# Kernel tuning notes

Measured on AMD Instinct MI355X. Metric: run time of the kernel, lower is better.

## Reference

```python
import jax, jax.numpy as jnp
import numpy as np

B, NT, NC, NN = 2, 64, 1024, 1024
C, H = 1024, 16
HD = C // H
N = NT + NC + NN
EPS = 1e-5
NEG = -1e30


def _ln(t, w, b):
    # LayerNorm over last dim (head_dim), torch eps=1e-5
    mu = jnp.mean(t, axis=-1, keepdims=True)
    var = jnp.mean(jnp.square(t - mu), axis=-1, keepdims=True)
    return (t - mu) * jax.lax.rsqrt(var + EPS) * w + b


def _rope(q, k, pos):
    # q,k: [B,H,S,HD]; pos: [B,S]; rotate-half RoPE, base 10000
    hd = q.shape[-1]
    half = hd // 2
    inv_freq = 1.0 / (10000.0 ** (jnp.arange(half, dtype=jnp.float32) / half))
    ang = pos.astype(jnp.float32)[:, None, :, None] * inv_freq  # [B,1,S,half]
    cos, sin = jnp.cos(ang), jnp.sin(ang)
    def rot(t):
        t1, t2 = t[..., :half], t[..., half:]
        return jnp.concatenate([t1 * cos - t2 * sin, t2 * cos + t1 * sin], axis=-1)
    return rot(q), rot(k)


def setup_inputs() -> dict:
    key = jax.random.key(0)
    ks = jax.random.split(key, 4)
    s = 0.02
    return {
        "x": jax.random.normal(ks[0], (B, N, C), jnp.float32),
        "position_ids": jnp.broadcast_to(jnp.arange(NC + NN, dtype=jnp.int32), (B, NC + NN)),
        "text_position_ids": jnp.broadcast_to(jnp.arange(NT, dtype=jnp.int32), (B, NT)),
        "attention_mask": jnp.tril(jnp.ones((N, N), dtype=bool)),
        "n_text": NT, "n_clean": NC, "n_noised": NN,
        "qkv_w": jax.random.normal(ks[1], (3, 3 * C, C), jnp.float32) * s,
        "qkv_b": jnp.zeros((3, 3 * C), jnp.float32),
        "qn_w": jnp.ones((3, HD), jnp.float32),
        "qn_b": jnp.zeros((3, HD), jnp.float32),
        "kn_w": jnp.ones((3, HD), jnp.float32),
        "kn_b": jnp.zeros((3, HD), jnp.float32),
        "proj_w": jax.random.normal(ks[2], (3, C, C), jnp.float32) * s,
        "proj_b": jnp.zeros((3, C), jnp.float32),
    }


def reference(x, position_ids, text_position_ids, attention_mask, n_text, n_clean, n_noised,
              qkv_w, qkv_b, qn_w, qn_b, kn_w, kn_b, proj_w, proj_b):
    Bx, Nx, Cx = x.shape
    hd = qn_w.shape[-1]
    nh = Cx // hd
    b0, b1 = n_text, n_text + n_clean
    segs = (x[:, :b0], x[:, b0:b1], x[:, b1:])  # text / clean / noised

    qs, kks, vvs = [], [], []
    for i, xs in enumerate(segs):
        S = xs.shape[1]
        qkv = jnp.einsum('bsc,oc->bso', xs, qkv_w[i]) + qkv_b[i]
        qkv = qkv.reshape(Bx, S, 3, nh, hd).transpose(2, 0, 3, 1, 4)  # [3,B,H,S,hd]
        q = _ln(qkv[0], qn_w[i], qn_b[i])
        k = _ln(qkv[1], kn_w[i], kn_b[i])
        qs.append(q); kks.append(k); vvs.append(qkv[2])

    img_q = jnp.concatenate([qs[1], qs[2]], axis=2)
    img_k = jnp.concatenate([kks[1], kks[2]], axis=2)
    img_q, img_k = _rope(img_q, img_k, position_ids)
    txt_q, txt_k = _rope(qs[0], kks[0], text_position_ids)

    q = jnp.concatenate([txt_q, img_q], axis=2)
    k = jnp.concatenate([txt_k, img_k], axis=2)
    v = jnp.concatenate(vvs, axis=2)

    scale = 1.0 / np.sqrt(hd).astype(np.float32)
    scores = jnp.einsum('bhqd,bhkd->bhqk', q, k) * scale
    scores = jnp.where(attention_mask, scores, NEG)
    attn = jax.nn.softmax(scores, axis=-1)
    out = jnp.einsum('bhqk,bhkd->bhqd', attn, v)
    out = out.transpose(0, 2, 1, 3).reshape(Bx, Nx, Cx)

    o_segs = (out[:, :b0], out[:, b0:b1], out[:, b1:])
    outs = [jnp.einsum('bsc,oc->bso', o_segs[i], proj_w[i]) + proj_b[i] for i in range(3)]
    return jnp.concatenate(outs, axis=1)
```

## Files before the change

### kernel.cpp

```cpp
#include <hip/hip_runtime.h>
#include <hip/hip_bf16.h>

#define BB   2
#define NT   64
#define NC   1024
#define NN   1024
#define NTOK (NT + NC + NN)
#define CC   1024
#define HH   16
#define HD   64
#define K3   (3 * CC)
#define EPSV 1e-5f

typedef __attribute__((ext_vector_type(8))) short short8;
typedef __attribute__((ext_vector_type(4))) float f32x4;
typedef __attribute__((ext_vector_type(4))) float float4v;

__device__ __forceinline__ short bf16raw(float x) {
    __hip_bfloat16 h = __float2bfloat16(x);
    return *(short*)&h;
}

#define GL_LDS(gptr, lptr) \
    __builtin_amdgcn_global_load_lds( \
        (const __attribute__((address_space(1))) void*)(gptr), \
        (__attribute__((address_space(3))) void*)(lptr), 16, 0, 0)

__constant__ signed char QB_tab[33] =
    {16,16,16,15,15,15,14,14,14,13,13,13,12,12,12,11,11,10,10,9,9,8,8,7,7,6,6,5,4,3,2,1,0};
__constant__ signed char CH_tab[33] =
    { 0, 1, 2, 0, 1, 2, 0, 1, 2, 0, 1, 2, 0, 1, 2, 0, 1, 0, 1,0,1,0,1,0,1,0,1,0,0,0,0,0,0};

__global__ __launch_bounds__(256) void cast_all(
    const float* __restrict__ s0, const float* __restrict__ s1, const float* __restrict__ s2,
    __hip_bfloat16* __restrict__ d0, __hip_bfloat16* __restrict__ d1, __hip_bfloat16* __restrict__ d2,
    int n0, int n1, int n2)
{
    int i = blockIdx.x * 256 + threadIdx.x;
    int stride = gridDim.x * 256;
    int ntot = n0 + n1 + n2;
    for (; i < ntot; i += stride) {
        const float* sp; short* dp; int j;
        if (i < n0)            { sp = s0; dp = (short*)d0; j = i; }
        else if (i < n0 + n1)  { sp = s1; dp = (short*)d1; j = i - n0; }
        else                   { sp = s2; dp = (short*)d2; j = i - n0 - n1; }
        float4v v = *(const float4v*)(sp + (size_t)j * 4);
        short4 o;
        o.x = bf16raw(v.x); o.y = bf16raw(v.y); o.z = bf16raw(v.z); o.w = bf16raw(v.w);
        *(short4*)(dp + (size_t)j * 4) = o;
    }
}

__global__ __launch_bounds__(256) void gemm_qkv(
    const __hip_bfloat16* __restrict__ A,
    const __hip_bfloat16* __restrict__ Wb,
    const float* __restrict__ biasb,
    const float* __restrict__ qn_w, const float* __restrict__ qn_b,
    const float* __restrict__ kn_w, const float* __restrict__ kn_b,
    __hip_bfloat16* __restrict__ Q,
    __hip_bfloat16* __restrict__ Kg,
    __hip_bfloat16* __restrict__ Vt)
{
    __shared__ short buf[128 * 134];
    short* As = buf;
    short* Bs = buf + 8192;

    int tid = threadIdx.x;
    int lane = tid & 63, w = tid >> 6;
    int l15 = lane & 15, quad = lane >> 4;
    int wm = w >> 1, wn = w & 1;
    int r7 = l15 & 7;

    int y = blockIdx.y;
    int seg, tm;
    if (y < 16)      { seg = 1; tm = y * 128; }
    else if (y < 32) { seg = 2; tm = (y - 16) * 128; }
    else             { seg = 0; tm = 0; }
    int S = (seg == 0) ? 64 : 1024;
    int seg_start = (seg == 0) ? 0 : (seg == 1 ? NT : NT + NC);
    const short* W = (const short*)Wb + (size_t)seg * K3 * CC;
    const float* bias = biasb + (size_t)seg * K3;
    int tileN = blockIdx.x * 128;

    const short* aptr[4];
    const short* bptr[4];
#pragma unroll
    for (int j = 0; j < 4; ++j) {
        int c = j * 256 + tid;
        int row = c >> 3, u = (c & 7) ^ (row & 7);
        int ar = tm + row;
        int arow = (ar / S) * NTOK + seg_start + (ar % S);
        aptr[j] = (const short*)A + (size_t)arow * CC + u * 8;
        bptr[j] = W + (size_t)(tileN + row) * CC + u * 8;
    }

    f32x4 zero = {0.f, 0.f, 0.f, 0.f};
    f32x4 acc[4][4];
#pragma unroll
    for (int mb = 0; mb < 4; ++mb)
#pragma unroll
        for (int nb = 0; nb < 4; ++nb) acc[mb][nb] = zero;

    for (int k0 = 0; k0 < CC; k0 += 64) {
        __syncthreads();
#pragma unroll
        for (int j = 0; j < 4; ++j) {
            int c8 = (j * 256 + tid) * 8;
            GL_LDS(aptr[j] + k0, As + c8);
            GL_LDS(bptr[j] + k0, Bs + c8);
        }
        __syncthreads();

#pragma unroll
        for (int s = 0; s < 2; ++s) {
            int sx = ((s * 4 + quad) ^ r7) * 8;
            short8 af[4], bf[4];
#pragma unroll
            for (int mb = 0; mb < 4; ++mb)
                af[mb] = *(const short8*)&As[(wm * 64 + mb * 16 + l15) * 64 + sx];
#pragma unroll
            for (int nb = 0; nb < 4; ++nb)
                bf[nb] = *(const short8*)&Bs[(wn * 64 + nb * 16 + l15) * 64 + sx];
#pragma unroll
            for (int mb = 0; mb < 4; ++mb)
#pragma unroll
                for (int nb = 0; nb < 4; ++nb)
                    acc[mb][nb] = __builtin_amdgcn_mfma_f32_16x16x32_bf16(af[mb], bf[nb], acc[mb][nb], 0, 0, 0);
        }
    }

    int sect = tileN >> 10;
    __syncthreads();

    if (sect < 2) {
        const float* nw = (sect == 0 ? qn_w : kn_w) + seg * HD;
        const float* nbv = (sect == 0 ? qn_b : kn_b) + seg * HD;
        float lw[4], lb[4], bcol[4];
#pragma unroll
        for (int nb = 0; nb < 4; ++nb) {
            lw[nb] = nw[nb * 16 + l15];
            lb[nb] = nbv[nb * 16 + l15];
            bcol[nb] = bias[tileN + wn * 64 + nb * 16 + l15];
        }
        float qscale = (sect == 0) ? 0.125f : 1.0f;

        float invf0 = expf(-9.210340371976184f * (float)l15 * (1.0f / 32.0f));
        float invf1 = expf(-9.210340371976184f * (float)(16 + l15) * (1.0f / 32.0f));
        float cd0, sd0, cd1, sd1;
        sincosf(invf0, &sd0, &cd0);
        sincosf(invf1, &sd1, &cd1);

#pragma unroll
        for (int mb = 0; mb < 4; ++mb) {
            int tok0 = wm * 64 + mb * 16 + quad * 4;
            int ar0 = tm + tok0;
            int nloc0 = ar0 % S;
            int pos0 = (seg == 0) ? nloc0 : (seg_start + nloc0 - NT);
            float c0, s0, c1, s1v;
            sincosf((float)pos0 * invf0, &s0, &c0);
            sincosf((float)pos0 * invf1, &s1v, &c1);

#pragma unroll
            for (int r = 0; r < 4; ++r) {
                int tok = tok0 + r;
                float v[4];
#pragma unroll
                for (int nb = 0; nb < 4; ++nb) v[nb] = acc[mb][nb][r] + bcol[nb];

                float t1 = v[0] + v[1] + v[2] + v[3];
                float t2 = v[0] * v[0] + v[1] * v[1] + v[2] * v[2] + v[3] * v[3];
#pragma unroll
                for (int off = 8; off >= 1; off >>= 1) {
                    t1 += __shfl_xor(t1, off);
                    t2 += __shfl_xor(t2, off);
                }
                float mu = t1 * (1.0f / 64.0f);
                float var = t2 * (1.0f / 64.0f) - mu * mu;
                float rstd = rsqrtf(var + EPSV);
#pragma unroll
                for (int nb = 0; nb < 4; ++nb) v[nb] = (v[nb] - mu) * rstd * lw[nb] + lb[nb];

                short* bp = &buf[tok * 134 + wn * 64];
                bp[0 * 16 + l15] = bf16raw((v[0] * c0 - v[2] * s0) * qscale);
                bp[1 * 16 + l15] = bf16raw((v[1] * c1 - v[3] * s1v) * qscale);
                bp[2 * 16 + l15] = bf16raw((v[2] * c0 + v[0] * s0) * qscale);
                bp[3 * 16 + l15] = bf16raw((v[3] * c1 + v[1] * s1v) * qscale);

                float nc0 = c0 * cd0 - s0 * sd0, ns0 = s0 * cd0 + c0 * sd0;
                float nc1 = c1 * cd1 - s1v * sd1, ns1 = s1v * cd1 + c1 * sd1;
                c0 = nc0; s0 = ns0; c1 = nc1; s1v = ns1;
            }
        }
        __syncthreads();
        __hip_bfloat16* dst = (sect == 0) ? Q : Kg;
        int head_base = (tileN & 1023) >> 6;
#pragma unroll
        for (int it = 0; it < 8; ++it) {
            int idx = it * 256 + tid;
            int tok = idx >> 4, cc = (idx & 15) * 8;
            int ar = tm + tok;
            int bb = ar / S;
            int nloc = seg_start + (ar % S);
            int hh2 = head_base + (cc >> 6), d = cc & 63;
            *(short8*)((short*)dst + ((size_t)(bb * HH + hh2) * NTOK + nloc) * HD + d) =
                *(const short8*)&buf[tok * 134 + cc];
        }
    } else {
        float bcol[4];
#pragma unroll
        for (int nb = 0; nb < 4; ++nb) bcol[nb] = bias[tileN + wn * 64 + nb * 16 + l15];
#pragma unroll
        for (int mb = 0; mb < 4; ++mb) {
#pragma unroll
            for (int r = 0; r < 4; ++r) {
                int tok = wm * 64 + mb * 16 + quad * 4 + r;
#pragma unroll
                for (int nb = 0; nb < 4; ++nb) {
                    int col = wn * 64 + nb * 16 + l15;
                    buf[col * 134 + tok] = bf16raw(acc[mb][nb][r] + bcol[nb]);
                }
            }
        }
        __syncthreads();
#pragma unroll
        for (int it = 0; it < 8; ++it) {
            int idx = it * 256 + tid;
            int row = idx >> 4;
            int tc = (idx & 15) * 8;
            int vcol = (tileN - 2048) + row;
            int h = vcol >> 6, d = vcol & 63;
            int ar = tm + tc;
            int bb = ar / S;
            int nloc = seg_start + (ar % S);
            short8 val = *(const short8*)&buf[row * 134 + tc];
            *(short8*)((short*)Vt + ((size_t)(bb * HH + h) * HD + d) * NTOK + nloc) = val;
        }
    }
}

__global__ __launch_bounds__(256) void gemm_proj(
    const __hip_bfloat16* __restrict__ A,
    const __hip_bfloat16* __restrict__ Wb,
    const float* __restrict__ biasb,
    float* __restrict__ Cout)
{
    __shared__ short As[64 * 64];
    __shared__ short Bs[128 * 64];

    int tid = threadIdx.x;
    int lane = tid & 63, w = tid >> 6;
    int l15 = lane & 15, quad = lane >> 4;
    int wm = w >> 1, wn = w & 1;
    int r7 = l15 & 7;

    int y = blockIdx.y;
    int seg, tm;
    if (y < 32)      { seg = 1; tm = y * 64; }
    else if (y < 64) { seg = 2; tm = (y - 32) * 64; }
    else             { seg = 0; tm = (y - 64) * 64; }
    int S = (seg == 0) ? 64 : 1024;
    int seg_start = (seg == 0) ? 0 : (seg == 1 ? NT : NT + NC);
    const short* W = (const short*)Wb + (size_t)seg * CC * CC;
    const float* bias = biasb + (size_t)seg * CC;
    int tileN = blockIdx.x * 128;

    const short* aptr[2];
    const short* bptr[4];
#pragma unroll
    for (int j = 0; j < 2; ++j) {
        int c = j * 256 + tid;
        int row = c >> 3, u = (c & 7) ^ (row & 7);
        int ar = tm + row;
        int arow = (ar / S) * NTOK + seg_start + (ar % S);
        aptr[j] = (const short*)A + (size_t)arow * CC + u * 8;
    }
#pragma unroll
    for (int j = 0; j < 4; ++j) {
        int c = j * 256 + tid;
        int row = c >> 3, u = (c & 7) ^ (row & 7);
        bptr[j] = W + (size_t)(tileN + row) * CC + u * 8;
    }

    f32x4 zero = {0.f, 0.f, 0.f, 0.f};
    f32x4 acc[2][4];
#pragma unroll
    for (int mb = 0; mb < 2; ++mb)
#pragma unroll
        for (int nb = 0; nb < 4; ++nb) acc[mb][nb] = zero;

    for (int k0 = 0; k0 < CC; k0 += 64) {
        __syncthreads();
#pragma unroll
        for (int j = 0; j < 2; ++j)
            GL_LDS(aptr[j] + k0, As + (j * 256 + tid) * 8);
#pragma unroll
        for (int j = 0; j < 4; ++j)
            GL_LDS(bptr[j] + k0, Bs + (j * 256 + tid) * 8);
        __syncthreads();

#pragma unroll
        for (int s = 0; s < 2; ++s) {
            int sx = ((s * 4 + quad) ^ r7) * 8;
            short8 af[2], bf[4];
#pragma unroll
            for (int mb = 0; mb < 2; ++mb)
                af[mb] = *(const short8*)&As[(wm * 32 + mb * 16 + l15) * 64 + sx];
#pragma unroll
            for (int nb = 0; nb < 4; ++nb)
                bf[nb] = *(const short8*)&Bs[(wn * 64 + nb * 16 + l15) * 64 + sx];
#pragma unroll
            for (int mb = 0; mb < 2; ++mb)
#pragma unroll
                for (int nb = 0; nb < 4; ++nb)
                    acc[mb][nb] = __builtin_amdgcn_mfma_f32_16x16x32_bf16(af[mb], bf[nb], acc[mb][nb], 0, 0, 0);
        }
    }

#pragma unroll
    for (int mb = 0; mb < 2; ++mb) {
#pragma unroll
        for (int r = 0; r < 4; ++r) {
            int ar = tm + wm * 32 + mb * 16 + quad * 4 + r;
            int crow = (ar / S) * NTOK + seg_start + (ar % S);
            float* cp = Cout + (size_t)crow * CC + tileN;
#pragma unroll
            for (int nb = 0; nb < 4; ++nb) {
                int col = wn * 64 + nb * 16 + l15;
                cp[col] = acc[mb][nb][r] + bias[tileN + col];
            }
        }
    }
}

__global__ __launch_bounds__(512) void attn_part(
    const __hip_bfloat16* __restrict__ Q,
    const __hip_bfloat16* __restrict__ Kg,
    const __hip_bfloat16* __restrict__ Vt,
    __hip_bfloat16* __restrict__ O,
    float* __restrict__ Opart,
    float* __restrict__ lpart)
{
    __shared__ short Ks[64 * 64];
    __shared__ short Vs[64 * 64];
    __shared__ short Ps[8][16 * 72];

    int tid = threadIdx.x;
    int lane = tid & 63, w = tid >> 6;
    int quad = lane >> 4, l15 = lane & 15;
    int r7 = l15 & 7;
    int bh = blockIdx.y, b = bh >> 4, h = bh & 15;

    int e = blockIdx.x;
    int qb = QB_tab[e], c = CH_tab[e];
    int q0 = qb * 128;
    int nt = 2 * qb + 2; if (nt > 33) nt = 33;
    int t0 = c * 12, t1 = t0 + 12; if (t1 > nt) t1 = nt;
    bool direct = (nt <= 12);

    size_t base = (size_t)bh * NTOK * HD;

    int qrow = q0 + w * 16 + l15;
    int qr_c = qrow < NTOK ? qrow : NTOK - 1;
    short8 qf0 = *(const short8*)((const short*)Q + base + (size_t)qr_c * HD + quad * 8);
    short8 qf1 = *(const short8*)((const short*)Q + base + (size_t)qr_c * HD + 32 + quad * 8);

    int srow = tid >> 3;
    int su = (tid & 7) ^ (srow & 7);
    const short* kptr = (const short*)Kg + base + (size_t)srow * HD + su * 8;
    const short* vptr = (const short*)Vt + base + (size_t)srow * NTOK + su * 8;
    int c8 = tid * 8;

    f32x4 zero = {0.f, 0.f, 0.f, 0.f};
    f32x4 oacc[4] = {zero, zero, zero, zero};
    float l[4] = {0.f, 0.f, 0.f, 0.f};

    int qmax_w = q0 + w * 16 + 15;
    int sx0 = (quad ^ r7) * 8;
    int sx1 = ((4 + quad) ^ r7) * 8;

    for (int t = t0; t < t1; ++t) {
        __syncthreads();
        GL_LDS(kptr + (size_t)(t * 64) * HD, Ks + c8);
        GL_LDS(vptr + t * 64, Vs + c8);
        __syncthreads();
        if (t * 64 > qmax_w) continue;

        f32x4 s[4];
#pragma unroll
        for (int kb = 0; kb < 4; ++kb) {
            int krow = (kb * 16 + l15) * 64;
            short8 kf0 = *(const short8*)&Ks[krow + sx0];
            short8 kf1 = *(const short8*)&Ks[krow + sx1];
            f32x4 z = zero;
            z = __builtin_amdgcn_mfma_f32_16x16x32_bf16(qf0, kf0, z, 0, 0, 0);
            z = __builtin_amdgcn_mfma_f32_16x16x32_bf16(qf1, kf1, z, 0, 0, 0);
            s[kb] = z;
        }

#pragma unroll
        for (int r = 0; r < 4; ++r) {
            int qg = q0 + w * 16 + quad * 4 + r;
#pragma unroll
            for (int kb = 0; kb < 4; ++kb) {
                int kgk = t * 64 + kb * 16 + l15;
                float p = (kgk <= qg) ? __expf(s[kb][r]) : 0.f;
                Ps[w][(quad * 4 + r) * 72 + kb * 16 + l15] = bf16raw(p);
                l[r] += p;
            }
        }

        __builtin_amdgcn_wave_barrier();

#pragma unroll
        for (int sl = 0; sl < 2; ++sl) {
            short8 pf = *(const short8*)&Ps[w][l15 * 72 + sl * 32 + quad * 8];
            int vsx = ((sl * 4 + quad) ^ r7) * 8;
#pragma unroll
            for (int db = 0; db < 4; ++db) {
                short8 vf = *(const short8*)&Vs[(db * 16 + l15) * 64 + vsx];
                oacc[db] = __builtin_amdgcn_mfma_f32_16x16x32_bf16(pf, vf, oacc[db], 0, 0, 0);
            }
        }
    }

#pragma unroll
    for (int r = 0; r < 4; ++r) {
#pragma unroll
        for (int off = 8; off >= 1; off >>= 1) l[r] += __shfl_xor(l[r], off);
    }

    if (direct) {
#pragma unroll
        for (int r = 0; r < 4; ++r) {
            int qg = q0 + w * 16 + quad * 4 + r;
            float inv_l = 1.0f / l[r];
#pragma unroll
            for (int db = 0; db < 4; ++db) {
                O[(size_t)(b * NTOK + qg) * CC + h * HD + db * 16 + l15] =
                    __float2bfloat16(oacc[db][r] * inv_l);
            }
        }
    } else {
        int pidx = (bh * 17 + qb) * 3 + c;
        float* op = Opart + (size_t)pidx * (128 * 64);
#pragma unroll
        for (int r = 0; r < 4; ++r) {
            int q = w * 16 + quad * 4 + r;
#pragma unroll
            for (int db = 0; db < 4; ++db)
                op[q * 64 + db * 16 + l15] = oacc[db][r];
            if (l15 == 0) lpart[pidx * 128 + q] = l[r];
        }
    }
}

__global__ __launch_bounds__(512) void attn_comb(
    const float* __restrict__ Opart, const float* __restrict__ lpart,
    __hip_bfloat16* __restrict__ O)
{
    __shared__ float ls[128];
    int tid = threadIdx.x;
    int qb = 6 + blockIdx.x;
    int bh = blockIdx.y, b = bh >> 4, h = bh & 15;
    int nt = 2 * qb + 2; if (nt > 33) nt = 33;
    int nch = (nt + 11) / 12;
    int q0 = qb * 128;
    int pbase = (bh * 17 + qb) * 3;

    if (tid < 128) {
        float s = 0.f;
        for (int cc = 0; cc < nch; ++cc) s += lpart[(pbase + cc) * 128 + tid];
        ls[tid] = 1.0f / s;
    }
    __syncthreads();

#pragma unroll
    for (int k = 0; k < 16; ++k) {
        int elem = k * 512 + tid;
        int q = elem >> 6, d = elem & 63;
        int qg = q0 + q;
        if (qg >= NTOK) continue;
        float s = 0.f;
        for (int cc = 0; cc < nch; ++cc)
            s += Opart[(size_t)(pbase + cc) * (128 * 64) + elem];
        O[(size_t)(b * NTOK + qg) * CC + h * HD + d] = __float2bfloat16(s * ls[q]);
    }
}

extern "C" void kernel_launch(void* const* d_in, const int* in_sizes, int n_in,
                              void* d_out, int out_size, void* d_ws, size_t ws_size,
                              hipStream_t stream) {
    const float* x      = (const float*)d_in[0];
    const float* qkv_w  = (const float*)d_in[7];
    const float* qkv_b  = (const float*)d_in[8];
    const float* qn_w   = (const float*)d_in[9];
    const float* qn_b   = (const float*)d_in[10];
    const float* kn_w   = (const float*)d_in[11];
    const float* kn_b   = (const float*)d_in[12];
    const float* proj_w = (const float*)d_in[13];
    const float* proj_b = (const float*)d_in[14];
    float* out = (float*)d_out;

    const size_t n_x    = (size_t)BB * NTOK * CC;
    const size_t n_qkvw = (size_t)3 * K3 * CC;
    const size_t n_prjw = (size_t)3 * CC * CC;
    const size_t n_part = (size_t)32 * 17 * 3;

    __hip_bfloat16* x_bf    = (__hip_bfloat16*)d_ws;
    __hip_bfloat16* qkvw_bf = x_bf + n_x;
    __hip_bfloat16* prjw_bf = qkvw_bf + n_qkvw;
    __hip_bfloat16* Qbf  = prjw_bf + n_prjw;
    __hip_bfloat16* Kbf  = Qbf + n_x;
    __hip_bfloat16* Vtbf = Kbf + n_x;
    float* Opart = (float*)(Vtbf + n_x);
    float* lpart = Opart + n_part * (128 * 64);
    __hip_bfloat16* attn_bf = x_bf;

    cast_all<<<1024, 256, 0, stream>>>(x, qkv_w, proj_w, x_bf, qkvw_bf, prjw_bf,
                                       (int)(n_x / 4), (int)(n_qkvw / 4), (int)(n_prjw / 4));

    gemm_qkv<<<dim3(K3 / 128, 33), 256, 0, stream>>>(
        x_bf, qkvw_bf, qkv_b,
        qn_w, qn_b, kn_w, kn_b, Qbf, Kbf, Vtbf);

    attn_part<<<dim3(33, BB * HH), 512, 0, stream>>>(Qbf, Kbf, Vtbf, attn_bf, Opart, lpart);

    attn_comb<<<dim3(11, BB * HH), 512, 0, stream>>>(Opart, lpart, attn_bf);

    gemm_proj<<<dim3(CC / 128, 66), 256, 0, stream>>>(attn_bf, prjw_bf, proj_b, out);
}
```

Baseline: 270.6 us.

## Double-buffer LDS tiles in QKV, projection and attention kernels

Adds ping-pong LDS buffers to the QKV GEMM, projection GEMM and attention loop. The next K-tile (or K/V block) is issued with global_load_lds before computing on the current one, and the two barriers per iteration become one. This is meant to hide global-load latency behind MFMA work. LDS use doubles per block, which may lower occupancy, most notably in the QKV GEMM at 64KB.

```diff
diff --git a/kernel.cpp b/kernel.cpp
--- a/kernel.cpp
+++ b/kernel.cpp
@@ -61,9 +61,8 @@
     __hip_bfloat16* __restrict__ Kg,
     __hip_bfloat16* __restrict__ Vt)
 {
-    __shared__ short buf[128 * 134];
-    short* As = buf;
-    short* Bs = buf + 8192;
+    __shared__ short lds[32768];
+    short* buf = lds;
 
     int tid = threadIdx.x;
     int lane = tid & 63, w = tid >> 6;
@@ -101,15 +100,27 @@
 #pragma unroll
         for (int nb = 0; nb < 4; ++nb) acc[mb][nb] = zero;
 
-    for (int k0 = 0; k0 < CC; k0 += 64) {
-        __syncthreads();
-#pragma unroll
-        for (int j = 0; j < 4; ++j) {
-            int c8 = (j * 256 + tid) * 8;
-            GL_LDS(aptr[j] + k0, As + c8);
-            GL_LDS(bptr[j] + k0, Bs + c8);
-        }
-        __syncthreads();
+#pragma unroll
+    for (int j = 0; j < 4; ++j) {
+        int c8 = (j * 256 + tid) * 8;
+        GL_LDS(aptr[j], lds + c8);
+        GL_LDS(bptr[j], lds + 8192 + c8);
+    }
+    __syncthreads();
+
+    int cur = 0;
+    for (int k0 = 64; k0 <= CC; k0 += 64) {
+        short* As = lds + cur * 16384;
+        short* Bs = As + 8192;
+        if (k0 < CC) {
+            short* An = lds + (cur ^ 1) * 16384;
+#pragma unroll
+            for (int j = 0; j < 4; ++j) {
+                int c8 = (j * 256 + tid) * 8;
+                GL_LDS(aptr[j] + k0, An + c8);
+                GL_LDS(bptr[j] + k0, An + 8192 + c8);
+            }
+        }
 
 #pragma unroll
         for (int s = 0; s < 2; ++s) {
@@ -127,10 +138,11 @@
                 for (int nb = 0; nb < 4; ++nb)
                     acc[mb][nb] = __builtin_amdgcn_mfma_f32_16x16x32_bf16(af[mb], bf[nb], acc[mb][nb], 0, 0, 0);
         }
+        __syncthreads();
+        cur ^= 1;
     }
 
     int sect = tileN >> 10;
-    __syncthreads();
 
     if (sect < 2) {
         const float* nw = (sect == 0 ? qn_w : kn_w) + seg * HD;
@@ -244,8 +256,7 @@
     const float* __restrict__ biasb,
     float* __restrict__ Cout)
 {
-    __shared__ short As[64 * 64];
-    __shared__ short Bs[128 * 64];
+    __shared__ short lds[24576];
 
     int tid = threadIdx.x;
     int lane = tid & 63, w = tid >> 6;
@@ -288,15 +299,27 @@
 #pragma unroll
         for (int nb = 0; nb < 4; ++nb) acc[mb][nb] = zero;
 
-    for (int k0 = 0; k0 < CC; k0 += 64) {
-        __syncthreads();
-#pragma unroll
-        for (int j = 0; j < 2; ++j)
-            GL_LDS(aptr[j] + k0, As + (j * 256 + tid) * 8);
-#pragma unroll
-        for (int j = 0; j < 4; ++j)
-            GL_LDS(bptr[j] + k0, Bs + (j * 256 + tid) * 8);
-        __syncthreads();
+#pragma unroll
+    for (int j = 0; j < 2; ++j)
+        GL_LDS(aptr[j], lds + (j * 256 + tid) * 8);
+#pragma unroll
+    for (int j = 0; j < 4; ++j)
+        GL_LDS(bptr[j], lds + 4096 + (j * 256 + tid) * 8);
+    __syncthreads();
+
+    int cur = 0;
+    for (int k0 = 64; k0 <= CC; k0 += 64) {
+        short* As = lds + cur * 12288;
+        short* Bs = As + 4096;
+        if (k0 < CC) {
+            short* An = lds + (cur ^ 1) * 12288;
+#pragma unroll
+            for (int j = 0; j < 2; ++j)
+                GL_LDS(aptr[j] + k0, An + (j * 256 + tid) * 8);
+#pragma unroll
+            for (int j = 0; j < 4; ++j)
+                GL_LDS(bptr[j] + k0, An + 4096 + (j * 256 + tid) * 8);
+        }
 
 #pragma unroll
         for (int s = 0; s < 2; ++s) {
@@ -314,6 +337,8 @@
                 for (int nb = 0; nb < 4; ++nb)
                     acc[mb][nb] = __builtin_amdgcn_mfma_f32_16x16x32_bf16(af[mb], bf[nb], acc[mb][nb], 0, 0, 0);
         }
+        __syncthreads();
+        cur ^= 1;
     }
 
 #pragma unroll
@@ -340,8 +365,8 @@
     float* __restrict__ Opart,
     float* __restrict__ lpart)
 {
-    __shared__ short Ks[64 * 64];
-    __shared__ short Vs[64 * 64];
+    __shared__ short Ks[2][4096];
+    __shared__ short Vs[2][4096];
     __shared__ short Ps[8][16 * 72];
 
     int tid = threadIdx.x;
@@ -378,49 +403,58 @@
     int sx0 = (quad ^ r7) * 8;
     int sx1 = ((4 + quad) ^ r7) * 8;
 
+    GL_LDS(kptr + (size_t)(t0 * 64) * HD, Ks[0] + c8);
+    GL_LDS(vptr + t0 * 64, Vs[0] + c8);
+    __syncthreads();
+
+    int cur = 0;
     for (int t = t0; t < t1; ++t) {
+        if (t + 1 < t1) {
+            GL_LDS(kptr + (size_t)((t + 1) * 64) * HD, Ks[cur ^ 1] + c8);
+            GL_LDS(vptr + (t + 1) * 64, Vs[cur ^ 1] + c8);
+        }
+
+        if (t * 64 <= qmax_w) {
+            f32x4 s[4];
+#pragma unroll
+            for (int kb = 0; kb < 4; ++kb) {
+                int krow = (kb * 16 + l15) * 64;
+                short8 kf0 = *(const short8*)&Ks[cur][krow + sx0];
+                short8 kf1 = *(const short8*)&Ks[cur][krow + sx1];
+                f32x4 z = zero;
+                z = __builtin_amdgcn_mfma_f32_16x16x32_bf16(qf0, kf0, z, 0, 0, 0);
+                z = __builtin_amdgcn_mfma_f32_16x16x32_bf16(qf1, kf1, z, 0, 0, 0);
+                s[kb] = z;
+            }
+
+#pragma unroll
+            for (int r = 0; r < 4; ++r) {
+                int qg = q0 + w * 16 + quad * 4 + r;
+#pragma unroll
+                for (int kb = 0; kb < 4; ++kb) {
+                    int kgk = t * 64 + kb * 16 + l15;
+                    float p = (kgk <= qg) ? __expf(s[kb][r]) : 0.f;
+                    Ps[w][(quad * 4 + r) * 72 + kb * 16 + l15] = bf16raw(p);
+                    l[r] += p;
+                }
+            }
+
+            __builtin_amdgcn_wave_barrier();
+
+#pragma unroll
+            for (int sl = 0; sl < 2; ++sl) {
+                short8 pf = *(const short8*)&Ps[w][l15 * 72 + sl * 32 + quad * 8];
+                int vsx = ((sl * 4 + quad) ^ r7) * 8;
+#pragma unroll
+                for (int db = 0; db < 4; ++db) {
+                    short8 vf = *(const short8*)&Vs[cur][(db * 16 + l15) * 64 + vsx];
+                    oacc[db] = __builtin_amdgcn_mfma_f32_16x16x32_bf16(pf, vf, oacc[db], 0, 0, 0);
+                }
+            }
+        }
+
         __syncthreads();
-        GL_LDS(kptr + (size_t)(t * 64) * HD, Ks + c8);
-        GL_LDS(vptr + t * 64, Vs + c8);
-        __syncthreads();
-        if (t * 64 > qmax_w) continue;
-
-        f32x4 s[4];
-#pragma unroll
-        for (int kb = 0; kb < 4; ++kb) {
-            int krow = (kb * 16 + l15) * 64;
-            short8 kf0 = *(const short8*)&Ks[krow + sx0];
-            short8 kf1 = *(const short8*)&Ks[krow + sx1];
-            f32x4 z = zero;
-            z = __builtin_amdgcn_mfma_f32_16x16x32_bf16(qf0, kf0, z, 0, 0, 0);
-            z = __builtin_amdgcn_mfma_f32_16x16x32_bf16(qf1, kf1, z, 0, 0, 0);
-            s[kb] = z;
-        }
-
-#pragma unroll
-        for (int r = 0; r < 4; ++r) {
-            int qg = q0 + w * 16 + quad * 4 + r;
-#pragma unroll
-            for (int kb = 0; kb < 4; ++kb) {
-                int kgk = t * 64 + kb * 16 + l15;
-                float p = (kgk <= qg) ? __expf(s[kb][r]) : 0.f;
-                Ps[w][(quad * 4 + r) * 72 + kb * 16 + l15] = bf16raw(p);
-                l[r] += p;
-            }
-        }
-
-        __builtin_amdgcn_wave_barrier();
-
-#pragma unroll
-        for (int sl = 0; sl < 2; ++sl) {
-            short8 pf = *(const short8*)&Ps[w][l15 * 72 + sl * 32 + quad * 8];
-            int vsx = ((sl * 4 + quad) ^ r7) * 8;
-#pragma unroll
-            for (int db = 0; db < 4; ++db) {
-                short8 vf = *(const short8*)&Vs[(db * 16 + l15) * 64 + vsx];
-                oacc[db] = __builtin_amdgcn_mfma_f32_16x16x32_bf16(pf, vf, oacc[db], 0, 0, 0);
-            }
-        }
+        cur ^= 1;
     }
 
 #pragma unroll
```

After: 264.8 us. 1.02x faster.
